# Optimization experiments

Measured on AMD Instinct MI355X. Metric: run time of the kernel, lower is better.

Reference implementation:

```python
import jax, jax.numpy as jnp
import numpy as np

D_MODEL = 1024
NUM_HEADS = 16
D_K = D_MODEL // NUM_HEADS
B, S = 4, 2048


def setup_inputs() -> dict:
    key = jax.random.key(0)
    ks = jax.random.split(key, 12)
    scale = 1.0 / np.sqrt(D_MODEL)
    inp = {
        "q": jax.random.normal(ks[0], (B, S, D_MODEL), dtype=jnp.float32),
        "k": jax.random.normal(ks[1], (B, S, D_MODEL), dtype=jnp.float32),
        "v": jax.random.normal(ks[2], (B, S, D_MODEL), dtype=jnp.float32),
        "mask": jnp.ones((B, 1, 1, S), dtype=jnp.int32),
        "Wq": jax.random.normal(ks[3], (D_MODEL, D_MODEL), dtype=jnp.float32) * scale,
        "bq": jnp.zeros((D_MODEL,), dtype=jnp.float32),
        "Wk": jax.random.normal(ks[4], (D_MODEL, D_MODEL), dtype=jnp.float32) * scale,
        "bk": jnp.zeros((D_MODEL,), dtype=jnp.float32),
        "Wv": jax.random.normal(ks[5], (D_MODEL, D_MODEL), dtype=jnp.float32) * scale,
        "bv": jnp.zeros((D_MODEL,), dtype=jnp.float32),
        "Wo": jax.random.normal(ks[6], (D_MODEL, D_MODEL), dtype=jnp.float32) * scale,
        "bo": jnp.zeros((D_MODEL,), dtype=jnp.float32),
    }
    return inp


def reference(q, k, v, mask, Wq, bq, Wk, bk, Wv, bv, Wo, bo):
    b, s, d = q.shape
    # QKV projections (torch Linear: x @ W.T + b; here weights stored as (d,d) used as x @ W + b)
    query = (q @ Wq + bq).reshape(b, s, NUM_HEADS, D_K).transpose(0, 2, 1, 3)  # (b,h,s,dk)
    key_ = (k @ Wk + bk).reshape(b, s, NUM_HEADS, D_K).transpose(0, 2, 1, 3)
    value = (v @ Wv + bv).reshape(b, s, NUM_HEADS, D_K).transpose(0, 2, 1, 3)
    # full score matrix (b,h,s,s), scaled by sqrt(d_k)
    scores = jnp.einsum("bhqd,bhkd->bhqk", query, key_) / jnp.sqrt(jnp.float32(D_K))
    scores = jnp.where(mask == 0, jnp.float32(-jnp.inf), scores)
    attn = jax.nn.softmax(scores, axis=-1)
    # dropout p=0.0 (eval) -> identity
    out = jnp.einsum("bhqk,bhkd->bhqd", attn, value)  # (b,h,s,dk)
    out = out.transpose(0, 2, 1, 3).reshape(b, s, NUM_HEADS * D_K)
    return out @ Wo + bo
```

## Files before the change

kernel.cpp:

```cpp
#include <hip/hip_runtime.h>

typedef __attribute__((ext_vector_type(8)))  short  short8;
typedef __attribute__((ext_vector_type(4)))  short  short4v;
typedef __attribute__((ext_vector_type(4)))  float  f32x4;
typedef __attribute__((ext_vector_type(16))) float  f32x16;
typedef __attribute__((ext_vector_type(8)))  __bf16 bf8_t;
typedef __attribute__((ext_vector_type(4)))  __bf16 bf4_t;

#define DMODEL 1024
#define SEQ    2048
#define NB     4
#define NH     16
#define MTOT   (NB * SEQ)
#define SCALE_LOG2E 0.18033688011112042f

static __device__ __forceinline__ ushort f2bf(float f) {
  union { float f; unsigned u; } v; v.f = f;
  unsigned r = v.u + 0x7fffu + ((v.u >> 16) & 1u);
  return (ushort)(r >> 16);
}

static __device__ __forceinline__ float fexp2(float x) {
#if __has_builtin(__builtin_amdgcn_exp2f)
  return __builtin_amdgcn_exp2f(x);
#else
  return __expf(x * 0.6931471805599453f);
#endif
}

static __device__ __forceinline__ f32x4 mfma32(short8 a, short8 b, f32x4 c) {
  return __builtin_amdgcn_mfma_f32_16x16x32_bf16(
      __builtin_bit_cast(bf8_t, a), __builtin_bit_cast(bf8_t, b), c, 0, 0, 0);
}

static __device__ __forceinline__ f32x16 mfma3232(short8 a, short8 b, f32x16 c) {
  return __builtin_amdgcn_mfma_f32_32x32x16_bf16(
      __builtin_bit_cast(bf8_t, a), __builtin_bit_cast(bf8_t, b), c, 0, 0, 0);
}

static __device__ __forceinline__ f32x16 mfma3208(short4v a, short4v b, f32x16 c) {
#if __has_builtin(__builtin_amdgcn_mfma_f32_32x32x8bf16_1k)
  return __builtin_amdgcn_mfma_f32_32x32x8bf16_1k(a, b, c, 0, 0, 0);
#else
  asm volatile("v_mfma_f32_32x32x8_bf16 %0, %1, %2, %0" : "+v"(c) : "v"(a), "v"(b));
  return c;
#endif
}

static __device__ __forceinline__ short4v pk4(float a, float b, float c, float d) {
  bf4_t t; t[0] = (__bf16)a; t[1] = (__bf16)b; t[2] = (__bf16)c; t[3] = (__bf16)d;
  return __builtin_bit_cast(short4v, t);
}

static __device__ __forceinline__ void gl_lds16(const ushort* g, ushort* l) {
  __builtin_amdgcn_global_load_lds(
      (const __attribute__((address_space(1))) unsigned*)(unsigned long long)g,
      (__attribute__((address_space(3))) unsigned*)(unsigned long long)l,
      16, 0, 0);
}

__global__ __launch_bounds__(256) void cvt_k(const float* __restrict__ src,
                                             ushort* __restrict__ dst) {
  const size_t i = ((size_t)blockIdx.x * 256 + threadIdx.x) * 8;
  const float4 a0 = *(const float4*)&src[i];
  const float4 a1 = *(const float4*)&src[i + 4];
  bf8_t c;
  c[0] = (__bf16)a0.x; c[1] = (__bf16)a0.y; c[2] = (__bf16)a0.z; c[3] = (__bf16)a0.w;
  c[4] = (__bf16)a1.x; c[5] = (__bf16)a1.y; c[6] = (__bf16)a1.z; c[7] = (__bf16)a1.w;
  *(short8*)&dst[i] = __builtin_bit_cast(short8, c);
}

__global__ __launch_bounds__(64) void bias_k(const int* __restrict__ mask,
                                             float* __restrict__ biasf,
                                             unsigned* __restrict__ flags) {
  const int t = blockIdx.x * 64 + threadIdx.x;
  const int m = mask[t];
  biasf[t] = m ? 0.f : -1e30f;
  const unsigned long long bal = __ballot(m == 0);
  if (threadIdx.x == 0) flags[blockIdx.x] = (bal != 0ull) ? 1u : 0u;
}

__global__ __launch_bounds__(1024) void wtrans_k(
    const float* __restrict__ Wq, const float* __restrict__ Wk,
    const float* __restrict__ Wv, const float* __restrict__ Wo,
    ushort* __restrict__ Wt) {
  __shared__ float tile[32][33];
  const int z = blockIdx.z;
  const float* W = (z == 0) ? Wq : (z == 1) ? Wk : (z == 2) ? Wv : Wo;
  ushort* out = Wt + (size_t)z * DMODEL * DMODEL;
  const int tx = threadIdx.x, ty = threadIdx.y;
  const int n0 = blockIdx.x * 32, k0 = blockIdx.y * 32;
  tile[ty][tx] = W[(size_t)(k0 + ty) * DMODEL + n0 + tx];
  __syncthreads();
  out[(size_t)(n0 + ty) * DMODEL + k0 + tx] = f2bf(tile[tx][ty]);
}

template <int MODE>
__global__ __launch_bounds__(256) void gemm_k(
    const ushort* __restrict__ A, const ushort* __restrict__ Bt,
    const float* __restrict__ bias, void* __restrict__ out, const float scale) {
  __shared__ ushort Asm[128 * 32];
  __shared__ ushort Bsm[128 * 32];
  const int tid = threadIdx.x;
  const int wid = tid >> 6, lane = tid & 63;
  const int wr = wid >> 1, wc = wid & 1;
  const int lr = lane & 15, lg = lane >> 4;
  const int m0 = blockIdx.x * 128, n0 = blockIdx.y * 128;

  const int srow = lane >> 2, sslot = (lane & 3) * 8;
  const size_t gA0 = (size_t)(m0 + wid * 16 + srow) * DMODEL + sslot;
  const size_t gA1 = (size_t)(m0 + (wid + 4) * 16 + srow) * DMODEL + sslot;
  const size_t gB0 = (size_t)(n0 + wid * 16 + srow) * DMODEL + sslot;
  const size_t gB1 = (size_t)(n0 + (wid + 4) * 16 + srow) * DMODEL + sslot;
  ushort* lA0 = &Asm[wid * 512];
  ushort* lA1 = &Asm[(wid + 4) * 512];
  ushort* lB0 = &Bsm[wid * 512];
  ushort* lB1 = &Bsm[(wid + 4) * 512];

  f32x4 acc[4][4];
#pragma unroll
  for (int m = 0; m < 4; m++)
#pragma unroll
    for (int n = 0; n < 4; n++) acc[m][n] = (f32x4){0.f, 0.f, 0.f, 0.f};

  gl_lds16(&A[gA0], lA0);
  gl_lds16(&A[gA1], lA1);
  gl_lds16(&Bt[gB0], lB0);
  gl_lds16(&Bt[gB1], lB1);

  for (int ks = 0; ks < DMODEL / 32; ++ks) {
    __syncthreads();

    short8 af[4], bfr[4];
#pragma unroll
    for (int m = 0; m < 4; m++)
      af[m] = *(const short8*)&Asm[(wr * 64 + m * 16 + lr) * 32 + lg * 8];
#pragma unroll
    for (int n = 0; n < 4; n++)
      bfr[n] = *(const short8*)&Bsm[(wc * 64 + n * 16 + lr) * 32 + lg * 8];
#pragma unroll
    for (int m = 0; m < 4; m++)
#pragma unroll
      for (int n = 0; n < 4; n++) acc[m][n] = mfma32(af[m], bfr[n], acc[m][n]);

    __syncthreads();
    if (ks < DMODEL / 32 - 1) {
      const size_t ko = (size_t)(ks + 1) * 32;
      gl_lds16(&A[gA0 + ko], lA0);
      gl_lds16(&A[gA1 + ko], lA1);
      gl_lds16(&Bt[gB0 + ko], lB0);
      gl_lds16(&Bt[gB1 + ko], lB1);
    }
  }

  float bv4[4];
#pragma unroll
  for (int n = 0; n < 4; n++) bv4[n] = bias[n0 + wc * 64 + n * 16 + lr];
#pragma unroll
  for (int m = 0; m < 4; m++) {
    const int grb = m0 + wr * 64 + m * 16 + lg * 4;
#pragma unroll
    for (int n = 0; n < 4; n++) {
      const int gc = n0 + wc * 64 + n * 16 + lr;
      if (MODE == 2) {
        const int bb = grb >> 11, ss = grb & 2047, hh = gc >> 6, dk = gc & 63;
        bf4_t pk;
#pragma unroll
        for (int j = 0; j < 4; j++) pk[j] = (__bf16)((acc[m][n][j] + bv4[n]) * scale);
        const size_t addr = (((size_t)bb * NH + hh) * SEQ) * 64 +
                            (size_t)(ss >> 6) * 4096 + dk * 64 +
                            ((ss & 63) ^ ((dk & 7) * 8));
        *(short4v*)&((ushort*)out)[addr] = __builtin_bit_cast(short4v, pk);
      } else {
#pragma unroll
        for (int j = 0; j < 4; j++) {
          float val = (acc[m][n][j] + bv4[n]) * scale;
          int r = grb + j;
          if (MODE == 0) {
            int b = r >> 11, s = r & 2047, hh = gc >> 6, dk = gc & 63;
            ((ushort*)out)[((((size_t)b * NH + hh) * SEQ) + s) * 64 + dk] =
                __builtin_bit_cast(ushort, (__bf16)val);
          } else if (MODE == 3) {
            int b = r >> 11, s = r & 2047, hh = gc >> 6, dk = gc & 63;
            const size_t addr = (((size_t)b * NH + hh) * SEQ) * 64 +
                                (size_t)(s >> 6) * 4096 + (s & 63) * 64 +
                                (dk ^ ((s & 7) * 8));
            ((ushort*)out)[addr] = __builtin_bit_cast(ushort, (__bf16)val);
          } else {
            ((float*)out)[(size_t)r * DMODEL + gc] = val;
          }
        }
      }
    }
  }
}

__global__ __launch_bounds__(256) void attn_k(
    const ushort* __restrict__ Qp, const ushort* __restrict__ Kp,
    const ushort* __restrict__ Vt, const float* __restrict__ biasf,
    const unsigned* __restrict__ flags, ushort* __restrict__ ctx) {
  __shared__ ushort smem[16384];
  const int tid = threadIdx.x, w = tid >> 6, lane = tid & 63;
  const int q = lane & 31, hi = lane >> 5;
  const int n = blockIdx.x;
  const int xcd = n & 7, idx = n >> 3;
  const int bh = ((idx >> 4) << 3) | xcd;
  const int qt = idx & 15;
  const int b = bh >> 4, h = bh & 15;
  const int q0w = qt * 128 + w * 32;
  const ushort* Qh = Qp + (size_t)bh * SEQ * 64;
  const ushort* Kh = Kp + (size_t)bh * SEQ * 64;
  const ushort* Vh = Vt + (size_t)bh * SEQ * 64;
  const float* biasb = biasf + b * SEQ;
  const unsigned* flb = flags + b * 32;

  short8 qf[4];
#pragma unroll
  for (int c = 0; c < 4; c++)
    qf[c] = *(const short8*)&Qh[(size_t)(q0w + q) * 64 + c * 16 + hi * 8];

  const int xo = (q & 7) * 8;
  int koff[2][4];
#pragma unroll
  for (int c = 0; c < 4; c++) {
    koff[0][c] = q * 64 + ((c * 16 + hi * 8) ^ xo);
    koff[1][c] = koff[0][c] + 32 * 64;
  }
  int voff[8];
#pragma unroll
  for (int g = 0; g < 8; g++)
    voff[g] = q * 64 + ((g * 8) ^ xo) + hi * 4;

  const int sl = lane * 8;

  f32x16 o0, o1;
#pragma unroll
  for (int r = 0; r < 16; r++) { o0[r] = 0.f; o1[r] = 0.f; }
  float l_run = 0.f;

  gl_lds16(&Kh[w * 512 + sl], &smem[w * 512]);
  gl_lds16(&Kh[(w + 4) * 512 + sl], &smem[(w + 4) * 512]);
  gl_lds16(&Vh[w * 512 + sl], &smem[8192 + w * 512]);
  gl_lds16(&Vh[(w + 4) * 512 + sl], &smem[8192 + (w + 4) * 512]);
  __syncthreads();

  for (int it = 0; it < 32; ++it) {
    const int cur = it & 1;
    if (it < 31) {
      const size_t tb = (size_t)(it + 1) * 4096;
      ushort* kd = &smem[(cur ^ 1) * 4096];
      ushort* vd = &smem[8192 + (cur ^ 1) * 4096];
      gl_lds16(&Kh[tb + w * 512 + sl], &kd[w * 512]);
      gl_lds16(&Kh[tb + (w + 4) * 512 + sl], &kd[(w + 4) * 512]);
      gl_lds16(&Vh[tb + w * 512 + sl], &vd[w * 512]);
      gl_lds16(&Vh[tb + (w + 4) * 512 + sl], &vd[(w + 4) * 512]);
    }

    const ushort* kl = &smem[cur * 4096];
    const ushort* vl = &smem[8192 + cur * 4096];

    f32x16 s0, s1;
#pragma unroll
    for (int r = 0; r < 16; r++) { s0[r] = 0.f; s1[r] = 0.f; }
#pragma unroll
    for (int c = 0; c < 4; c++)
      s0 = mfma3232(*(const short8*)&kl[koff[0][c]], qf[c], s0);
#pragma unroll
    for (int c = 0; c < 4; c++)
      s1 = mfma3232(*(const short8*)&kl[koff[1][c]], qf[c], s1);

    float p[32];
#pragma unroll
    for (int r = 0; r < 16; r++) { p[r] = s0[r]; p[16 + r] = s1[r]; }

    if (flb[it]) {
      const float* bp = biasb + it * 64;
#pragma unroll
      for (int kt = 0; kt < 2; kt++)
#pragma unroll
        for (int g = 0; g < 4; g++) {
          const f32x4 ba = *(const f32x4*)&bp[kt * 32 + g * 8 + hi * 4];
#pragma unroll
          for (int j = 0; j < 4; j++) p[kt * 16 + g * 4 + j] += ba[j];
        }
    }

#pragma unroll
    for (int r = 0; r < 32; r++) p[r] = fexp2(p[r]);

    float a16[16], a8[8], a4[4];
#pragma unroll
    for (int i = 0; i < 16; i++) a16[i] = p[i] + p[16 + i];
#pragma unroll
    for (int i = 0; i < 8; i++) a8[i] = a16[i] + a16[8 + i];
#pragma unroll
    for (int i = 0; i < 4; i++) a4[i] = a8[i] + a8[4 + i];
    float ps = (a4[0] + a4[1]) + (a4[2] + a4[3]);
    ps += __shfl_xor(ps, 32);
    l_run += ps;

    short4v pf[8];
#pragma unroll
    for (int g = 0; g < 4; g++)
      pf[g] = pk4(p[4 * g], p[4 * g + 1], p[4 * g + 2], p[4 * g + 3]);
#pragma unroll
    for (int g = 0; g < 4; g++)
      pf[4 + g] = pk4(p[16 + 4 * g], p[16 + 4 * g + 1], p[16 + 4 * g + 2],
                      p[16 + 4 * g + 3]);

#pragma unroll
    for (int g = 0; g < 8; g++) {
      const short4v va = *(const short4v*)&vl[voff[g]];
      const short4v vb = *(const short4v*)&vl[voff[g] + 2048];
      o0 = mfma3208(va, pf[g], o0);
      o1 = mfma3208(vb, pf[g], o1);
    }

    __syncthreads();
  }

  const float inv = 1.f / l_run;
  ushort* ow = &smem[w * 2176];
#pragma unroll
  for (int r = 0; r < 16; r++) {
    const int dk = (r & 3) + 8 * (r >> 2) + 4 * hi;
    ow[q * 68 + dk] = __builtin_bit_cast(ushort, (__bf16)(o0[r] * inv));
    ow[q * 68 + 32 + dk] = __builtin_bit_cast(ushort, (__bf16)(o1[r] * inv));
  }
  __syncthreads();
  const int sr = lane >> 4, dc = (lane & 15) * 4;
#pragma unroll
  for (int i = 0; i < 8; i++) {
    const int qq = i * 4 + sr;
    const short4v vv = *(const short4v*)&ow[qq * 68 + dc];
    *(short4v*)&ctx[((size_t)b * SEQ + q0w + qq) * DMODEL + h * 64 + dc] = vv;
  }
}

extern "C" void kernel_launch(void* const* d_in, const int* in_sizes, int n_in,
                              void* d_out, int out_size, void* d_ws,
                              size_t ws_size, hipStream_t stream) {
  const float* q    = (const float*)d_in[0];
  const float* k    = (const float*)d_in[1];
  const float* v    = (const float*)d_in[2];
  const int*   mask = (const int*)d_in[3];
  const float* Wq   = (const float*)d_in[4];
  const float* bq   = (const float*)d_in[5];
  const float* Wk   = (const float*)d_in[6];
  const float* bk   = (const float*)d_in[7];
  const float* Wv   = (const float*)d_in[8];
  const float* bv   = (const float*)d_in[9];
  const float* Wo   = (const float*)d_in[10];
  const float* bo   = (const float*)d_in[11];

  char* p = (char*)d_ws;
  ushort* Wt = (ushort*)p; p += (size_t)4 * DMODEL * DMODEL * 2;
  ushort* Qp = (ushort*)p; p += (size_t)MTOT * DMODEL * 2;
  ushort* Kp = (ushort*)p; p += (size_t)MTOT * DMODEL * 2;
  ushort* Vb = (ushort*)p; p += (size_t)MTOT * DMODEL * 2;
  ushort* qb = (ushort*)p; p += (size_t)MTOT * DMODEL * 2;
  ushort* kb = (ushort*)p; p += (size_t)MTOT * DMODEL * 2;
  ushort* vb = (ushort*)p; p += (size_t)MTOT * DMODEL * 2;
  float*  biasf = (float*)p; p += (size_t)NB * SEQ * 4;
  unsigned* flags = (unsigned*)p;
  ushort* ctx = qb;

  wtrans_k<<<dim3(32, 32, 4), dim3(32, 32), 0, stream>>>(Wq, Wk, Wv, Wo, Wt);
  bias_k<<<NB * SEQ / 64, 64, 0, stream>>>(mask, biasf, flags);
  cvt_k<<<MTOT * DMODEL / (256 * 8), 256, 0, stream>>>(q, qb);
  cvt_k<<<MTOT * DMODEL / (256 * 8), 256, 0, stream>>>(k, kb);
  cvt_k<<<MTOT * DMODEL / (256 * 8), 256, 0, stream>>>(v, vb);

  dim3 gg(MTOT / 128, DMODEL / 128);
  gemm_k<0><<<gg, 256, 0, stream>>>(qb, Wt, bq, Qp, SCALE_LOG2E);
  gemm_k<3><<<gg, 256, 0, stream>>>(kb, Wt + (size_t)DMODEL * DMODEL, bk, Kp, 1.f);
  gemm_k<2><<<gg, 256, 0, stream>>>(vb, Wt + (size_t)2 * DMODEL * DMODEL, bv, Vb, 1.f);

  attn_k<<<1024, 256, 0, stream>>>(Qp, Kp, Vb, biasf, flags, ctx);

  gemm_k<1><<<gg, 256, 0, stream>>>(ctx, Wt + (size_t)3 * DMODEL * DMODEL, bo,
                                    d_out, 1.f);
}
```

Before: 237.9 us.

## Use 32x32x16 MFMA for PV via permlane swap, pad LDS, merge convert kernels

The attention P·V product now uses the wider 32x32x16 bf16 MFMA instead of 32x32x8. The probability fragments are repacked across lane halves with v_permlane32_swap. The K/V LDS tiles get padded row chunks (stride 544) so K and V share one offset scheme and bank conflicts are reduced. The bias add is fused with exp2, and the three fp32→bf16 conversion launches are merged into one grid. This halves the PV MFMA instruction count and cuts launch overhead, at the cost of extra permlane instructions and more careful layout assumptions about the V tile.

```diff
diff --git a/kernel.cpp b/kernel.cpp
--- a/kernel.cpp
+++ b/kernel.cpp
@@ -6,6 +6,8 @@
 typedef __attribute__((ext_vector_type(16))) float  f32x16;
 typedef __attribute__((ext_vector_type(8)))  __bf16 bf8_t;
 typedef __attribute__((ext_vector_type(4)))  __bf16 bf4_t;
+typedef __attribute__((ext_vector_type(2)))  __bf16 bf2_t;
+typedef __attribute__((ext_vector_type(4)))  unsigned uint4v;
 
 #define DMODEL 1024
 #define SEQ    2048
@@ -13,6 +15,8 @@
 #define NH     16
 #define MTOT   (NB * SEQ)
 #define SCALE_LOG2E 0.18033688011112042f
+#define CSTRIDE 544
+#define TSPAN   (8 * CSTRIDE)
 
 static __device__ __forceinline__ ushort f2bf(float f) {
   union { float f; unsigned u; } v; v.f = f;
@@ -38,18 +42,13 @@
       __builtin_bit_cast(bf8_t, a), __builtin_bit_cast(bf8_t, b), c, 0, 0, 0);
 }
 
-static __device__ __forceinline__ f32x16 mfma3208(short4v a, short4v b, f32x16 c) {
-#if __has_builtin(__builtin_amdgcn_mfma_f32_32x32x8bf16_1k)
-  return __builtin_amdgcn_mfma_f32_32x32x8bf16_1k(a, b, c, 0, 0, 0);
-#else
-  asm volatile("v_mfma_f32_32x32x8_bf16 %0, %1, %2, %0" : "+v"(c) : "v"(a), "v"(b));
-  return c;
-#endif
-}
-
-static __device__ __forceinline__ short4v pk4(float a, float b, float c, float d) {
-  bf4_t t; t[0] = (__bf16)a; t[1] = (__bf16)b; t[2] = (__bf16)c; t[3] = (__bf16)d;
-  return __builtin_bit_cast(short4v, t);
+static __device__ __forceinline__ unsigned pk2(float a, float b) {
+  bf2_t t; t[0] = (__bf16)a; t[1] = (__bf16)b;
+  return __builtin_bit_cast(unsigned, t);
+}
+
+static __device__ __forceinline__ void plswap(unsigned& a, unsigned& b) {
+  asm volatile("v_permlane32_swap_b32 %0, %1" : "+v"(a), "+v"(b));
 }
 
 static __device__ __forceinline__ void gl_lds16(const ushort* g, ushort* l) {
@@ -59,8 +58,13 @@
       16, 0, 0);
 }
 
-__global__ __launch_bounds__(256) void cvt_k(const float* __restrict__ src,
-                                             ushort* __restrict__ dst) {
+__global__ __launch_bounds__(256) void cvt3_k(
+    const float* __restrict__ q, const float* __restrict__ k,
+    const float* __restrict__ v, ushort* __restrict__ qb,
+    ushort* __restrict__ kb, ushort* __restrict__ vb) {
+  const int z = blockIdx.y;
+  const float* src = (z == 0) ? q : (z == 1) ? k : v;
+  ushort* dst = (z == 0) ? qb : (z == 1) ? kb : vb;
   const size_t i = ((size_t)blockIdx.x * 256 + threadIdx.x) * 8;
   const float4 a0 = *(const float4*)&src[i];
   const float4 a1 = *(const float4*)&src[i + 4];
@@ -199,7 +203,7 @@
     const ushort* __restrict__ Qp, const ushort* __restrict__ Kp,
     const ushort* __restrict__ Vt, const float* __restrict__ biasf,
     const unsigned* __restrict__ flags, ushort* __restrict__ ctx) {
-  __shared__ ushort smem[16384];
+  __shared__ ushort smem[4 * TSPAN];
   const int tid = threadIdx.x, w = tid >> 6, lane = tid & 63;
   const int q = lane & 31, hi = lane >> 5;
   const int n = blockIdx.x;
@@ -220,59 +224,51 @@
     qf[c] = *(const short8*)&Qh[(size_t)(q0w + q) * 64 + c * 16 + hi * 8];
 
   const int xo = (q & 7) * 8;
-  int koff[2][4];
-#pragma unroll
-  for (int c = 0; c < 4; c++) {
-    koff[0][c] = q * 64 + ((c * 16 + hi * 8) ^ xo);
-    koff[1][c] = koff[0][c] + 32 * 64;
-  }
-  int voff[8];
-#pragma unroll
-  for (int g = 0; g < 8; g++)
-    voff[g] = q * 64 + ((g * 8) ^ xo) + hi * 4;
+  const int rbase = q * 64 + (q >> 3) * 32;
+  int off[4];
+#pragma unroll
+  for (int c = 0; c < 4; c++) off[c] = rbase + ((c * 16 + hi * 8) ^ xo);
 
   const int sl = lane * 8;
+  const int c0 = 2 * w, c1 = 2 * w + 1;
 
   f32x16 o0, o1;
 #pragma unroll
   for (int r = 0; r < 16; r++) { o0[r] = 0.f; o1[r] = 0.f; }
   float l_run = 0.f;
 
-  gl_lds16(&Kh[w * 512 + sl], &smem[w * 512]);
-  gl_lds16(&Kh[(w + 4) * 512 + sl], &smem[(w + 4) * 512]);
-  gl_lds16(&Vh[w * 512 + sl], &smem[8192 + w * 512]);
-  gl_lds16(&Vh[(w + 4) * 512 + sl], &smem[8192 + (w + 4) * 512]);
+  gl_lds16(&Kh[c0 * 512 + sl], &smem[c0 * CSTRIDE]);
+  gl_lds16(&Kh[c1 * 512 + sl], &smem[c1 * CSTRIDE]);
+  gl_lds16(&Vh[c0 * 512 + sl], &smem[2 * TSPAN + c0 * CSTRIDE]);
+  gl_lds16(&Vh[c1 * 512 + sl], &smem[2 * TSPAN + c1 * CSTRIDE]);
   __syncthreads();
 
   for (int it = 0; it < 32; ++it) {
     const int cur = it & 1;
     if (it < 31) {
       const size_t tb = (size_t)(it + 1) * 4096;
-      ushort* kd = &smem[(cur ^ 1) * 4096];
-      ushort* vd = &smem[8192 + (cur ^ 1) * 4096];
-      gl_lds16(&Kh[tb + w * 512 + sl], &kd[w * 512]);
-      gl_lds16(&Kh[tb + (w + 4) * 512 + sl], &kd[(w + 4) * 512]);
-      gl_lds16(&Vh[tb + w * 512 + sl], &vd[w * 512]);
-      gl_lds16(&Vh[tb + (w + 4) * 512 + sl], &vd[(w + 4) * 512]);
-    }
-
-    const ushort* kl = &smem[cur * 4096];
-    const ushort* vl = &smem[8192 + cur * 4096];
+      ushort* kd = &smem[(cur ^ 1) * TSPAN];
+      ushort* vd = &smem[2 * TSPAN + (cur ^ 1) * TSPAN];
+      gl_lds16(&Kh[tb + c0 * 512 + sl], &kd[c0 * CSTRIDE]);
+      gl_lds16(&Kh[tb + c1 * 512 + sl], &kd[c1 * CSTRIDE]);
+      gl_lds16(&Vh[tb + c0 * 512 + sl], &vd[c0 * CSTRIDE]);
+      gl_lds16(&Vh[tb + c1 * 512 + sl], &vd[c1 * CSTRIDE]);
+    }
+
+    const ushort* kl = &smem[cur * TSPAN];
+    const ushort* vl = &smem[2 * TSPAN + cur * TSPAN];
 
     f32x16 s0, s1;
 #pragma unroll
     for (int r = 0; r < 16; r++) { s0[r] = 0.f; s1[r] = 0.f; }
 #pragma unroll
     for (int c = 0; c < 4; c++)
-      s0 = mfma3232(*(const short8*)&kl[koff[0][c]], qf[c], s0);
+      s0 = mfma3232(*(const short8*)&kl[off[c]], qf[c], s0);
 #pragma unroll
     for (int c = 0; c < 4; c++)
-      s1 = mfma3232(*(const short8*)&kl[koff[1][c]], qf[c], s1);
+      s1 = mfma3232(*(const short8*)&kl[off[c] + 2176], qf[c], s1);
 
     float p[32];
-#pragma unroll
-    for (int r = 0; r < 16; r++) { p[r] = s0[r]; p[16 + r] = s1[r]; }
-
     if (flb[it]) {
       const float* bp = biasb + it * 64;
 #pragma unroll
@@ -281,12 +277,17 @@
         for (int g = 0; g < 4; g++) {
           const f32x4 ba = *(const f32x4*)&bp[kt * 32 + g * 8 + hi * 4];
 #pragma unroll
-          for (int j = 0; j < 4; j++) p[kt * 16 + g * 4 + j] += ba[j];
+          for (int j = 0; j < 4; j++)
+            p[kt * 16 + g * 4 + j] =
+                fexp2((kt ? s1[g * 4 + j] : s0[g * 4 + j]) + ba[j]);
         }
-    }
-
-#pragma unroll
-    for (int r = 0; r < 32; r++) p[r] = fexp2(p[r]);
+    } else {
+#pragma unroll
+      for (int r = 0; r < 16; r++) {
+        p[r] = fexp2(s0[r]);
+        p[16 + r] = fexp2(s1[r]);
+      }
+    }
 
     float a16[16], a8[8], a4[4];
 #pragma unroll
@@ -299,21 +300,22 @@
     ps += __shfl_xor(ps, 32);
     l_run += ps;
 
-    short4v pf[8];
-#pragma unroll
-    for (int g = 0; g < 4; g++)
-      pf[g] = pk4(p[4 * g], p[4 * g + 1], p[4 * g + 2], p[4 * g + 3]);
-#pragma unroll
-    for (int g = 0; g < 4; g++)
-      pf[4 + g] = pk4(p[16 + 4 * g], p[16 + 4 * g + 1], p[16 + 4 * g + 2],
-                      p[16 + 4 * g + 3]);
-
-#pragma unroll
-    for (int g = 0; g < 8; g++) {
-      const short4v va = *(const short4v*)&vl[voff[g]];
-      const short4v vb = *(const short4v*)&vl[voff[g] + 2048];
-      o0 = mfma3208(va, pf[g], o0);
-      o1 = mfma3208(vb, pf[g], o1);
+    short8 frag[4];
+#pragma unroll
+    for (int kb = 0; kb < 4; kb++) {
+      unsigned X0 = pk2(p[8 * kb + 0], p[8 * kb + 1]);
+      unsigned X1 = pk2(p[8 * kb + 2], p[8 * kb + 3]);
+      unsigned Y0 = pk2(p[8 * kb + 4], p[8 * kb + 5]);
+      unsigned Y1 = pk2(p[8 * kb + 6], p[8 * kb + 7]);
+      plswap(X0, Y0);
+      plswap(X1, Y1);
+      frag[kb] = __builtin_bit_cast(short8, (uint4v){X0, X1, Y0, Y1});
+    }
+
+#pragma unroll
+    for (int kb = 0; kb < 4; kb++) {
+      o0 = mfma3232(*(const short8*)&vl[off[kb]], frag[kb], o0);
+      o1 = mfma3232(*(const short8*)&vl[off[kb] + 2176], frag[kb], o1);
     }
 
     __syncthreads();
@@ -367,9 +369,8 @@
 
   wtrans_k<<<dim3(32, 32, 4), dim3(32, 32), 0, stream>>>(Wq, Wk, Wv, Wo, Wt);
   bias_k<<<NB * SEQ / 64, 64, 0, stream>>>(mask, biasf, flags);
-  cvt_k<<<MTOT * DMODEL / (256 * 8), 256, 0, stream>>>(q, qb);
-  cvt_k<<<MTOT * DMODEL / (256 * 8), 256, 0, stream>>>(k, kb);
-  cvt_k<<<MTOT * DMODEL / (256 * 8), 256, 0, stream>>>(v, vb);
+  cvt3_k<<<dim3(MTOT * DMODEL / (256 * 8), 3), 256, 0, stream>>>(q, k, v, qb,
+                                                                 kb, vb);
 
   dim3 gg(MTOT / 128, DMODEL / 128);
   gemm_k<0><<<gg, 256, 0, stream>>>(qb, Wt, bq, Qp, SCALE_LOG2E);
```

Result: faster. 231.2 us (-2.8%).
